# Optimization experiments

Hardware: AMD Instinct MI355X
Metric: run time of the kernel (lower is better)

Reference implementation:

```python
import jax, jax.numpy as jnp
import numpy as np

EPS = 1e-8

def squash(s, axis=-1):
    sq = jnp.sum(s * s, axis=axis, keepdims=True)
    return (sq / (1.0 + sq)) * s / jnp.sqrt(sq + EPS)

def conv3d(x, w, b, stride=1):
    y = jax.lax.conv_general_dilated(x, w, (stride,) * 3, 'VALID',
                                     dimension_numbers=('NCDHW', 'OIDHW', 'NCDHW'))
    return y + b[None, :, None, None, None]

def deconv3d(x, w, b, stride, pad, out_pad):
    # torch ConvTranspose3d: w is (Cin, Cout, k, k, k)
    k = w.shape[-1]
    wf = jnp.flip(w, axis=(2, 3, 4)).transpose(1, 0, 2, 3, 4)  # (Cout, Cin, k, k, k)
    pads = [(k - 1 - pad, k - 1 - pad + out_pad)] * 3
    y = jax.lax.conv_general_dilated(x, wf, (1, 1, 1), pads,
                                     lhs_dilation=(stride,) * 3,
                                     dimension_numbers=('NCDHW', 'OIDHW', 'NCDHW'))
    return y + b[None, :, None, None, None]

def voxel_ids(pcl, n):
    # per-cloud axis-aligned bounding box voxelization (PyntCloud voxelgrid semantics)
    mn = pcl.min(axis=1, keepdims=True)
    mx = pcl.max(axis=1, keepdims=True)
    idx = jnp.floor((pcl - mn) / (mx - mn + 1e-9) * n).astype(jnp.int32)
    idx = jnp.clip(idx, 0, n - 1)
    return idx[..., 0] * (n * n) + idx[..., 1] * n + idx[..., 2]  # (B, P) flat voxel id

def setup_inputs() -> dict:
    key = jax.random.key(0)
    ks = jax.random.split(key, 16)
    B, P, C, n = 2, 8192, 128, 24
    s = 0.02
    inp = {
        'pcl': jax.random.uniform(ks[0], (B, P, 3), jnp.float32),
        'pcl_feature': jax.random.normal(ks[1], (B, P, C), jnp.float32),
        'n': n,
        'conv1_w': jax.random.normal(ks[2], (256, 128, 5, 5, 5), jnp.float32) * s,
        'conv1_b': jnp.zeros((256,), jnp.float32),
        'conv2_w': jax.random.normal(ks[3], (256, 256, 5, 5, 5), jnp.float32) * s,
        'conv2_b': jnp.zeros((256,), jnp.float32),
        'prim_w': jax.random.normal(ks[4], (256, 256, 9, 9, 9), jnp.float32) * s,
        'prim_b': jnp.zeros((256,), jnp.float32),
        'route_w': jax.random.normal(ks[5], (50, 2048, 64, 8), jnp.float32) * s,
        'dec1_w': jax.random.normal(ks[6], (50, 128, 3, 3, 3), jnp.float32) * s,
        'dec1_b': jnp.zeros((128,), jnp.float32),
        'dec2_w': jax.random.normal(ks[7], (128, 512, 3, 3, 3), jnp.float32) * s,
        'dec2_b': jnp.zeros((512,), jnp.float32),
    }
    return inp

def reference(pcl, pcl_feature, n, conv1_w, conv1_b, conv2_w, conv2_b,
              prim_w, prim_b, route_w, dec1_w, dec1_b, dec2_w, dec2_b):
    B, P, C = pcl_feature.shape
    vid = voxel_ids(pcl, n)  # (B, P)
    # pcl2vox: scatter-add point features into dense voxel grid
    flat_ids = (jnp.arange(B)[:, None] * (n ** 3) + vid).reshape(-1)
    mesh = jax.ops.segment_sum(pcl_feature.reshape(B * P, C), flat_ids,
                               num_segments=B * n ** 3)
    mesh = mesh.reshape(B, n, n, n, C).transpose(0, 4, 1, 2, 3)  # (B, C, n, n, n)
    # conv encoder: 24 -> 20 -> 16
    h = jax.nn.relu(conv3d(mesh, conv1_w, conv1_b))
    h = jax.nn.relu(conv3d(h, conv2_w, conv2_b))  # (B, 256, 16, 16, 16)
    # primary capsules: k=9 s=2 -> (B, 256, 4, 4, 4) -> (B, 2048, 8), squash
    p = conv3d(h, prim_w, prim_b, stride=2)
    u = p.reshape(B, 32, 8, 64).transpose(0, 1, 3, 2).reshape(B, 2048, 8)
    u = squash(u)
    # dynamic routing: u_hat[b,j,i,d] = W[j,i,d,c] u[b,i,c]
    u_hat = jnp.einsum('jidc,bic->bjid', route_w, u)  # (B, 50, 2048, 64)
    b_log = jnp.zeros((B, 50, 2048), u_hat.dtype)
    n_iter = 1
    v = None
    for _ in range(n_iter):
        c = jax.nn.softmax(b_log, axis=1)
        s = jnp.einsum('bji,bjid->bjd', c, u_hat)
        v = squash(s)  # (B, 50, 64)
        b_log = b_log + jnp.einsum('bjid,bjd->bji', u_hat, v)
    # decoder: (B, 50, 4, 4, 4) -> (B, 128, 12^3) -> (B, 512, 24^3)
    r = v.reshape(B, 50, 4, 4, 4)
    d = jax.nn.relu(deconv3d(r, dec1_w, dec1_b, 3, 0, 0))
    d = jax.nn.relu(deconv3d(d, dec2_w, dec2_b, 2, 1, 1))  # (B, 512, 24, 24, 24)
    # vox2pcl: gather per-point features from voxel grid
    d_flat = d.reshape(B, 512, n ** 3)
    out = jnp.take_along_axis(d_flat, vid[:, None, :], axis=2)  # (B, 512, P)
    return out.transpose(0, 2, 1)  # (B, P, 512)
```

## Files before the change

### kernel.cpp

```cpp
#include <hip/hip_runtime.h>
#include <cstdint>
#include <cstddef>

typedef _Float16 h8 __attribute__((ext_vector_type(8)));
typedef _Float16 h4 __attribute__((ext_vector_type(4)));
typedef float    f32x4 __attribute__((ext_vector_type(4)));

#define B_   2
#define P_   8192
#define NVOX 24
#define N3   13824

#define MESHS_OFF 0ull
#define M16_OFF   14155776ull
#define H1CL_OFF  28311552ull
#define WB_OFF    44695552ull
#define WB2C_OFF  44695552ull
#define H2P_OFF   0ull
#define PPART_OFF 25165824ull
#define PR1_OFF   53477376ull
#define WBD_OFF   0ull
#define D2H_OFF   10616832ull
#define D1CL_OFF  38928384ull
#define VID_OFF   63504384ull
#define UBUF_OFF  63700992ull
#define SBUF_OFF  63832064ull
#define VBUF_OFF  63857664ull

#define M16_PL   3538944ull
#define H1_PL    4096000ull
#define D1_PL    442368ull

__device__ inline void split2(float x, _Float16& a0, _Float16& a1)
{
    a0 = (_Float16)x;
    float r = x - (float)a0;
    a1 = (_Float16)(r * 2048.0f);
}

__device__ inline void gload16(const void* g, void* l)
{
    __builtin_amdgcn_global_load_lds(
        (const __attribute__((address_space(1))) char*)g,
        (__attribute__((address_space(3))) char*)l, 16, 0, 0);
}

__device__ inline void tapDecode(int cls, int ti, int& kd, int& kh, int& kw)
{
    int px = (cls >> 2) & 1, py = (cls >> 1) & 1, pz = cls & 1;
    int tiz = pz ? (ti & 1) : 0;
    int t1  = ti >> pz;
    int tiy = py ? (t1 & 1) : 0;
    int tix = t1 >> py;
    kd = px ? tix*2 : 1;
    kh = py ? tiy*2 : 1;
    kw = pz ? tiz*2 : 1;
}

__global__ __launch_bounds__(256)
void k_vid(const float* __restrict__ pcl, int* __restrict__ vid)
{
    int b = blockIdx.x;
    const float* pb = pcl + (size_t)b * P_ * 3;
    float mn[3] = {3e38f, 3e38f, 3e38f};
    float mx[3] = {-3e38f, -3e38f, -3e38f};
    for (int p = threadIdx.x; p < P_; p += 256) {
        #pragma unroll
        for (int d = 0; d < 3; ++d) {
            float v = pb[p*3 + d];
            mn[d] = fminf(mn[d], v);
            mx[d] = fmaxf(mx[d], v);
        }
    }
    __shared__ float red[6][256];
    #pragma unroll
    for (int d = 0; d < 3; ++d) { red[d][threadIdx.x] = mn[d]; red[3+d][threadIdx.x] = mx[d]; }
    __syncthreads();
    for (int s = 128; s > 0; s >>= 1) {
        if (threadIdx.x < (unsigned)s) {
            #pragma unroll
            for (int d = 0; d < 3; ++d) {
                red[d][threadIdx.x]   = fminf(red[d][threadIdx.x],   red[d][threadIdx.x + s]);
                red[3+d][threadIdx.x] = fmaxf(red[3+d][threadIdx.x], red[3+d][threadIdx.x + s]);
            }
        }
        __syncthreads();
    }
    float mn0 = red[0][0], mn1 = red[1][0], mn2 = red[2][0];
    float dd0 = red[3][0] - mn0 + 1e-9f;
    float dd1 = red[4][0] - mn1 + 1e-9f;
    float dd2 = red[5][0] - mn2 + 1e-9f;
    for (int p = threadIdx.x; p < P_; p += 256) {
        float fx = (pb[p*3+0] - mn0) / dd0 * 24.0f;
        float fy = (pb[p*3+1] - mn1) / dd1 * 24.0f;
        float fz = (pb[p*3+2] - mn2) / dd2 * 24.0f;
        int ix = (int)floorf(fx); ix = ix < 0 ? 0 : (ix > 23 ? 23 : ix);
        int iy = (int)floorf(fy); iy = iy < 0 ? 0 : (iy > 23 ? 23 : iy);
        int iz = (int)floorf(fz); iz = iz < 0 ? 0 : (iz > 23 ? 23 : iz);
        vid[b*P_ + p] = ix*576 + iy*24 + iz;
    }
}

__global__ __launch_bounds__(256)
void k_scatter(const float* __restrict__ feat, const int* __restrict__ vid,
               float* __restrict__ meshS)
{
    int g = blockIdx.x*256 + threadIdx.x;
    int c  = g & 127;
    int bp = g >> 7;
    int v  = vid[bp];
    int b  = bp >> 13;
    atomicAdd(&meshS[((size_t)b*N3 + v)*128 + c], feat[g]);
}

__global__ __launch_bounds__(256)
void k_meshsplit(const float* __restrict__ meshS, _Float16* __restrict__ m16)
{
    int g = blockIdx.x*256 + threadIdx.x;
    int e = g*4;
    float4 a = *(const float4*)(meshS + e);
    h4 v0, v1;
    float xs[4] = {a.x, a.y, a.z, a.w};
    #pragma unroll
    for (int j = 0; j < 4; ++j) {
        _Float16 t0, t1; split2(xs[j], t0, t1);
        v0[j] = t0; v1[j] = t1;
    }
    *(h4*)(m16 + e)          = v0;
    *(h4*)(m16 + M16_PL + e) = v1;
}

__global__ __launch_bounds__(256)
void k_splitw1(const float* __restrict__ W, char* __restrict__ Wb)
{
    int g = blockIdx.x*256 + threadIdx.x;
    int el   = g & 8191;
    int tile = g >> 13;
    int m = tile / 250, c = tile - m*250;
    int co = el >> 6, kl = el & 63;
    int kg = c*64 + kl;
    int kid = kg >> 7, ci = kg & 127;
    float x = W[((size_t)((m*128 + co)*128 + ci))*125 + kid];
    _Float16 a0, a1; split2(x, a0, a1);
    char* dst = Wb + (size_t)tile*32768 + (co*128 + ((kl*2) ^ ((co&7)<<4)));
    *(_Float16*)(dst)         = a0;
    *(_Float16*)(dst + 16384) = a1;
}

__global__ __launch_bounds__(256)
void k_splitw2(const float* __restrict__ W, char* __restrict__ Wb, int cBase, int NC)
{
    int g = blockIdx.x*256 + threadIdx.x;
    int el   = g & 8191;
    int tile = g >> 13;
    int m = tile / NC, cl = tile - m*NC;
    int c = cBase + cl;
    int co = el >> 6, kl = el & 63;
    int kg = c*64 + kl;
    int kid = kg >> 8, ci = kg & 255;
    float x = W[((size_t)((m*128 + co)*256 + ci))*125 + kid];
    _Float16 a0, a1; split2(x, a0, a1);
    char* dst = Wb + (size_t)tile*32768 + (co*128 + ((kl*2) ^ ((co&7)<<4)));
    *(_Float16*)(dst)         = a0;
    *(_Float16*)(dst + 16384) = a1;
}

__global__ __launch_bounds__(256)
void k_splitwd2p(const float* __restrict__ W, char* __restrict__ Wb)
{
    int g = blockIdx.x*256 + threadIdx.x;
    int el   = g & 8191;
    int tile = g >> 13;
    int mG = tile / 54, chunkG = tile - mG*54;
    int co = el >> 6, kl = el & 63;
    int rem = chunkG, cls = 0;
    for (int c = 0; c < 8; ++c) {
        int cc = 2 << __popc(c);
        if (rem < cc) { cls = c; break; }
        rem -= cc;
    }
    int k  = rem*64 + kl;
    int ti = k >> 7;
    int ci = k & 127;
    int kd, kh, kw;
    tapDecode(cls, ti, kd, kh, kw);
    int kid = kd*9 + kh*3 + kw;
    float x = W[((size_t)ci*512 + (mG*128 + co))*27 + kid];
    _Float16 a0, a1; split2(x, a0, a1);
    char* dst = Wb + (size_t)tile*32768 + (co*128 + ((kl*2) ^ ((co&7)<<4)));
    *(_Float16*)(dst)         = a0;
    *(_Float16*)(dst + 16384) = a1;
}

__global__ __launch_bounds__(256, 3)
void k_conv1(const _Float16* __restrict__ m16, const char* __restrict__ Wb,
             const float* __restrict__ bias, _Float16* __restrict__ h1cl)
{
    extern __shared__ char lds[];
    const int tid = threadIdx.x;
    const int l   = tid & 63;
    const int w   = tid >> 6;
    const int wm  = w >> 1, wn = w & 1;
    const int n0  = blockIdx.x * 64;
    const int m   = blockIdx.y;

    const _Float16* preP[4];
    #pragma unroll
    for (int i = 0; i < 4; ++i) {
        int g   = w*4096 + i*1024 + l*16;
        int ver = g >> 13;
        int dd  = g & 8191;
        int nl  = dd >> 7;
        int lg  = (dd & 127) ^ ((nl & 7) << 4);
        int klocal = lg >> 1;
        int n  = n0 + nl;
        int b2 = n / 8000;
        int so = n - b2*8000;
        int x = so/400, y = (so/20)%20, z = so%20;
        preP[i] = m16 + (size_t)ver*M16_PL
                      + ((size_t)(b2*13824 + x*576 + y*24 + z))*128 + klocal;
    }

    const int swz = (l & 7) << 4;
    const int qo  = (l >> 4) << 4;
    const int plF = (l & 15)*128 + (qo ^ (swz & 0x30)) + (swz & 0x40);

    f32x4 acc0[4][2], acc1[4][2];
    const f32x4 zz = {0.f, 0.f, 0.f, 0.f};
    #pragma unroll
    for (int a = 0; a < 4; ++a)
        #pragma unroll
        for (int b = 0; b < 2; ++b) { acc0[a][b] = zz; acc1[a][b] = zz; }

    for (int c = 0; c < 250; ++c) {
        int kid = c >> 1;
        int kd = kid/25, rr = kid - kd*25, kh = rr/5, kw = rr - kh*5;
        int koff = (kd*576 + kh*24 + kw)*128 + (c & 1)*64;

        __syncthreads();
        {
            const char* wsrc = (const char*)Wb + ((size_t)(m*250 + c))*32768 + w*8192;
            #pragma unroll
            for (int i = 0; i < 8; ++i)
                gload16(wsrc + i*1024 + l*16, lds + w*8192 + i*1024);
            #pragma unroll
            for (int i = 0; i < 4; ++i)
                gload16(preP[i] + koff, lds + 32768 + w*4096 + i*1024);
        }
        __syncthreads();

        #pragma unroll
        for (int ks = 0; ks < 2; ++ks) {
            const int kx = ks ? 64 : 0;
            h8 af[2][4], bf[2][2];
            #pragma unroll
            for (int v = 0; v < 2; ++v) {
                #pragma unroll
                for (int mf = 0; mf < 4; ++mf)
                    af[v][mf] = *(const h8*)(lds + v*16384 + (wm*64 + mf*16)*128 + (plF ^ kx));
                #pragma unroll
                for (int nf = 0; nf < 2; ++nf)
                    bf[v][nf] = *(const h8*)(lds + 32768 + v*8192 + (wn*32 + nf*16)*128 + (plF ^ kx));
            }
            #pragma unroll
            for (int mf = 0; mf < 4; ++mf)
                #pragma unroll
                for (int nf = 0; nf < 2; ++nf) {
                    acc0[mf][nf] = __builtin_amdgcn_mfma_f32_16x16x32_f16(af[0][mf], bf[0][nf], acc0[mf][nf], 0,0,0);
                    acc1[mf][nf] = __builtin_amdgcn_mfma_f32_16x16x32_f16(af[0][mf], bf[1][nf], acc1[mf][nf], 0,0,0);
                    acc1[mf][nf] = __builtin_amdgcn_mfma_f32_16x16x32_f16(af[1][mf], bf[0][nf], acc1[mf][nf], 0,0,0);
                }
        }
    }

    const float s1 = 4.8828125e-04f;
    #pragma unroll
    for (int mf = 0; mf < 4; ++mf)
        #pragma unroll
        for (int nf = 0; nf < 2; ++nf) {
            f32x4 r = acc0[mf][nf] + s1*acc1[mf][nf];
            int co = m*128 + wm*64 + mf*16 + ((l>>4)<<2);
            int n  = n0 + wn*32 + nf*16 + (l&15);
            size_t base = (size_t)n*256 + co;
            h4 v0, v1;
            #pragma unroll
            for (int rr = 0; rr < 4; ++rr) {
                float x = fmaxf(r[rr] + bias[co + rr], 0.f);
                _Float16 t0, t1; split2(x, t0, t1);
                v0[rr] = t0; v1[rr] = t1;
            }
            *(h4*)(h1cl + base)         = v0;
            *(h4*)(h1cl + H1_PL + base) = v1;
        }
}

__global__ __launch_bounds__(256, 3)
void k_conv2(const _Float16* __restrict__ h1cl, const char* __restrict__ Wb,
             float* __restrict__ h2p, int cBase, int NSt, int accum)
{
    extern __shared__ char lds[];
    const int tid = threadIdx.x;
    const int l   = tid & 63;
    const int w   = tid >> 6;
    const int wm  = w >> 1, wn = w & 1;
    const int n0  = blockIdx.x * 64;
    const int m   = blockIdx.y;
    const int per = (NSt + (int)gridDim.z - 1) / (int)gridDim.z;
    const int cl0 = blockIdx.z * per;
    const int cl1 = min(NSt, cl0 + per);

    const _Float16* preP[4];
    #pragma unroll
    for (int i = 0; i < 4; ++i) {
        int g   = w*4096 + i*1024 + l*16;
        int ver = g >> 13;
        int dd  = g & 8191;
        int nl  = dd >> 7;
        int lg  = (dd & 127) ^ ((nl & 7) << 4);
        int klocal = lg >> 1;
        int n = n0 + nl;
        int b2 = n >> 12, so = n & 4095;
        int x = so >> 8, y = (so >> 4) & 15, z = so & 15;
        preP[i] = h1cl + (size_t)ver*H1_PL
                       + ((size_t)(b2*8000 + x*400 + y*20 + z))*256 + klocal;
    }

    const int swz = (l & 7) << 4;
    const int qo  = (l >> 4) << 4;
    const int plF = (l & 15)*128 + (qo ^ (swz & 0x30)) + (swz & 0x40);

    f32x4 acc0[4][2], acc1[4][2];
    const f32x4 zz = {0.f, 0.f, 0.f, 0.f};
    #pragma unroll
    for (int a = 0; a < 4; ++a)
        #pragma unroll
        for (int b = 0; b < 2; ++b) { acc0[a][b] = zz; acc1[a][b] = zz; }

    for (int cl = cl0; cl < cl1; ++cl) {
        int cg = cBase + cl;
        int kid = cg >> 2;
        int kd = kid/25, rr = kid - kd*25, kh = rr/5, kw = rr - kh*5;
        int koff = (kd*400 + kh*20 + kw)*256 + (cg & 3)*64;

        __syncthreads();
        {
            const char* wsrc = (const char*)Wb + ((size_t)(m*NSt + cl))*32768 + w*8192;
            #pragma unroll
            for (int i = 0; i < 8; ++i)
                gload16(wsrc + i*1024 + l*16, lds + w*8192 + i*1024);
            #pragma unroll
            for (int i = 0; i < 4; ++i)
                gload16(preP[i] + koff, lds + 32768 + w*4096 + i*1024);
        }
        __syncthreads();

        #pragma unroll
        for (int ks = 0; ks < 2; ++ks) {
            const int kx = ks ? 64 : 0;
            h8 af[2][4], bf[2][2];
            #pragma unroll
            for (int v = 0; v < 2; ++v) {
                #pragma unroll
                for (int mf = 0; mf < 4; ++mf)
                    af[v][mf] = *(const h8*)(lds + v*16384 + (wm*64 + mf*16)*128 + (plF ^ kx));
                #pragma unroll
                for (int nf = 0; nf < 2; ++nf)
                    bf[v][nf] = *(const h8*)(lds + 32768 + v*8192 + (wn*32 + nf*16)*128 + (plF ^ kx));
            }
            #pragma unroll
            for (int mf = 0; mf < 4; ++mf)
                #pragma unroll
                for (int nf = 0; nf < 2; ++nf) {
                    acc0[mf][nf] = __builtin_amdgcn_mfma_f32_16x16x32_f16(af[0][mf], bf[0][nf], acc0[mf][nf], 0,0,0);
                    acc1[mf][nf] = __builtin_amdgcn_mfma_f32_16x16x32_f16(af[0][mf], bf[1][nf], acc1[mf][nf], 0,0,0);
                    acc1[mf][nf] = __builtin_amdgcn_mfma_f32_16x16x32_f16(af[1][mf], bf[0][nf], acc1[mf][nf], 0,0,0);
                }
        }
    }

    const float s1 = 4.8828125e-04f;
    float* oz = h2p + (size_t)blockIdx.z * 2097152;
    #pragma unroll
    for (int mf = 0; mf < 4; ++mf)
        #pragma unroll
        for (int nf = 0; nf < 2; ++nf) {
            f32x4 r = acc0[mf][nf] + s1*acc1[mf][nf];
            int co = m*128 + wm*64 + mf*16 + ((l>>4)<<2);
            int n  = n0 + wn*32 + nf*16 + (l&15);
            int b2 = n >> 12, so = n & 4095;
            #pragma unroll
            for (int rr = 0; rr < 4; ++rr) {
                size_t idx = ((size_t)(b2*256 + co + rr))*4096 + so;
                if (accum) oz[idx] += r[rr];
                else       oz[idx]  = r[rr];
            }
        }
}

__global__ __launch_bounds__(256)
void k_h2epi(float* __restrict__ p0, const float* __restrict__ bias)
{
    int g = blockIdx.x*256 + threadIdx.x;
    int e = g*4;
    int co = (e >> 12) & 255;
    float4 a = *(const float4*)(p0 + e);
    float4 b = *(const float4*)(p0 + 2097152 + e);
    float4 c = *(const float4*)(p0 + 4194304 + e);
    float bb = bias[co];
    float4 r;
    r.x = fmaxf(a.x + b.x + c.x + bb, 0.f);
    r.y = fmaxf(a.y + b.y + c.y + bb, 0.f);
    r.z = fmaxf(a.z + b.z + c.z + bb, 0.f);
    r.w = fmaxf(a.w + b.w + c.w + bb, 0.f);
    *(float4*)(p0 + e) = r;
}

template<int CIN, int KD, int STRIDE, int IND, int OUTD>
__global__ __launch_bounds__(256, 2)
void k_gemm_conv(const float* __restrict__ in, const float* __restrict__ W,
                 float* __restrict__ out)
{
    constexpr int KD2  = KD*KD;
    constexpr int K3   = KD*KD*KD;
    constexpr int IND2 = IND*IND;
    constexpr int IND3 = IND2*IND;
    constexpr int OUT2 = OUTD*OUTD;
    constexpr int OUT3 = OUT2*OUTD;
    constexpr int KTOT = CIN*K3;
    constexpr int NCH  = KTOT/16;

    const int tid  = threadIdx.x;
    const int mIdx = tid >> 4;
    const int nIdx = tid & 15;
    const int n0   = blockIdx.x * 128;
    const int co0  = blockIdx.y * 128;
    const int per  = NCH / (int)gridDim.z;
    const int c0   = blockIdx.z * per;
    const int c1   = c0 + per;

    __shared__ float As[16][132];
    __shared__ float Bs[16][132];

    const int nB    = n0 + (tid & 127);
    const int kHalf = tid >> 7;
    int bB = nB / OUT3;
    int sB = nB - bB*OUT3;
    int xB = sB / OUT2;
    int yB = (sB / OUTD) % OUTD;
    int zB = sB % OUTD;
    const float* inB = in + (size_t)bB*CIN*IND3
                          + (xB*STRIDE)*IND2 + (yB*STRIDE)*IND + (zB*STRIDE);
    const int cB  = tid & 127;
    const int qB  = cB >> 2;
    const int bpos = ((((qB & 1) << 4) | (qB >> 1)) << 2) | (cB & 3);

    const int aCo = tid >> 2;
    const int aKq = (tid & 3) * 4;
    const int qA  = aCo >> 2;
    const int apos = ((((qA & 1) << 4) | (qA >> 1)) << 2) | (aCo & 3);
    const float* Wr0 = W + (size_t)(co0 + aCo)*KTOT + aKq;
    const float* Wr1 = W + (size_t)(co0 + 64 + aCo)*KTOT + aKq;

    float acc[8][8];
    #pragma unroll
    for (int i = 0; i < 8; ++i)
        #pragma unroll
        for (int j = 0; j < 8; ++j) acc[i][j] = 0.f;

    for (int c = c0; c < c1; ++c) {
        const int kb = c*16;
        float4 a0 = *(const float4*)(Wr0 + kb);
        float4 a1 = *(const float4*)(Wr1 + kb);
        float bv[8];
        #pragma unroll
        for (int p = 0; p < 8; ++p) {
            int k  = kb + p*2 + kHalf;
            int ci = k / K3;
            int r  = k - ci*K3;
            int kd = r / KD2;
            int r2 = r - kd*KD2;
            int kh = r2 / KD;
            int kw = r2 - kh*KD;
            bv[p] = inB[ci*IND3 + kd*IND2 + kh*IND + kw];
        }
        __syncthreads();
        As[aKq+0][apos] = a0.x; As[aKq+1][apos] = a0.y;
        As[aKq+2][apos] = a0.z; As[aKq+3][apos] = a0.w;
        As[aKq+0][apos+32] = a1.x; As[aKq+1][apos+32] = a1.y;
        As[aKq+2][apos+32] = a1.z; As[aKq+3][apos+32] = a1.w;
        #pragma unroll
        for (int p = 0; p < 8; ++p) Bs[p*2 + kHalf][bpos] = bv[p];
        __syncthreads();
        #pragma unroll
        for (int kk = 0; kk < 16; ++kk) {
            float af[8], bf[8];
            *(float4*)&af[0] = *(const float4*)&As[kk][mIdx*4];
            *(float4*)&af[4] = *(const float4*)&As[kk][64 + mIdx*4];
            *(float4*)&bf[0] = *(const float4*)&Bs[kk][nIdx*4];
            *(float4*)&bf[4] = *(const float4*)&Bs[kk][64 + nIdx*4];
            #pragma unroll
            for (int i = 0; i < 8; ++i)
                #pragma unroll
                for (int j = 0; j < 8; ++j)
                    acc[i][j] += af[i]*bf[j];
        }
    }

    float* oz = out + (size_t)blockIdx.z * (2*256*OUT3);
    #pragma unroll
    for (int j = 0; j < 8; ++j) {
        int n = n0 + nIdx*8 + j;
        int b = n / OUT3;
        int s = n - b*OUT3;
        float* o = oz + ((size_t)b*256 + co0 + mIdx*8)*OUT3 + s;
        #pragma unroll
        for (int i = 0; i < 8; ++i)
            o[(size_t)i*OUT3] = acc[i][j];
    }
}

__global__ __launch_bounds__(256)
void k_pr1(const float* __restrict__ pp, float* __restrict__ out1)
{
    int e = blockIdx.x*256 + threadIdx.x;
    int y = blockIdx.y;
    const float* src = pp + (size_t)y*27*32768 + e;
    float a = 0.f;
    #pragma unroll
    for (int j = 0; j < 27; ++j) a += src[(size_t)j*32768];
    out1[y*32768 + e] = a;
}

__global__ __launch_bounds__(256)
void k_pr2(const float* __restrict__ out1, const float* __restrict__ pbias,
           float* __restrict__ u)
{
    int g = blockIdx.x*256 + threadIdx.x;
    int b = g >> 11;
    int i = g & 2047;
    int cap = i >> 6;
    int s   = i & 63;
    float vals[8];
    float sq = 0.f;
    #pragma unroll
    for (int c = 0; c < 8; ++c) {
        size_t base = ((size_t)(b*256) + cap*8 + c)*64 + s;
        float a = 0.f;
        #pragma unroll
        for (int j = 0; j < 8; ++j) a += out1[(size_t)j*32768 + base];
        float x = a + pbias[cap*8 + c];
        vals[c] = x;
        sq += x*x;
    }
    float scale = (sq / (1.f + sq)) / sqrtf(sq + 1e-8f);
    #pragma unroll
    for (int c = 0; c < 8; ++c) u[(size_t)g*8 + c] = vals[c]*scale;
}

__global__ __launch_bounds__(256)
void k_route(const float* __restrict__ Wr, const float* __restrict__ u,
             float* __restrict__ s_buf)
{
    int j  = blockIdx.x;
    int i0 = blockIdx.y * 512;
    __shared__ float us[2*512*8];
    for (int idx = threadIdx.x; idx < 8192; idx += 256) {
        int b = idx >> 12;
        us[idx] = u[(size_t)b*16384 + (size_t)i0*8 + (idx & 4095)];
    }
    __syncthreads();
    int tid = threadIdx.x;
    int cc  = tid & 7;
    const float* Wj = Wr + (size_t)j*2048*512 + (size_t)i0*512;
    float a00 = 0.f, a01 = 0.f, a10 = 0.f, a11 = 0.f;
    for (int i = 0; i < 512; ++i) {
        float w0 = Wj[(size_t)i*512 + tid];
        float w1 = Wj[(size_t)i*512 + tid + 256];
        float u0 = us[i*8 + cc];
        float u1 = us[4096 + i*8 + cc];
        a00 += w0*u0; a01 += w1*u0; a10 += w0*u1; a11 += w1*u1;
    }
    __syncthreads();
    float* red = us;
    red[tid] = a00; red[256 + tid] = a01; red[512 + tid] = a10; red[768 + tid] = a11;
    __syncthreads();
    if (tid < 128) {
        int b = tid >> 6, d = tid & 63;
        const float* rb = red + b*512 + (d >> 5)*256 + (d & 31)*8;
        float s = 0.f;
        #pragma unroll
        for (int c2 = 0; c2 < 8; ++c2) s += rb[c2];
        atomicAdd(&s_buf[((size_t)b*50 + j)*64 + d], s * (1.0f/50.0f));
    }
}

__global__ __launch_bounds__(64)
void k_squash_v(const float* __restrict__ s_buf, float* __restrict__ v_buf)
{
    int row = blockIdx.x;
    int d   = threadIdx.x;
    float s  = s_buf[row*64 + d];
    float sq = s*s;
    #pragma unroll
    for (int o = 32; o > 0; o >>= 1) sq += __shfl_xor(sq, o);
    float scale = (sq / (1.f + sq)) / sqrtf(sq + 1e-8f);
    v_buf[row*64 + d] = s*scale;
}

__global__ __launch_bounds__(256)
void k_dec1(const float* __restrict__ v, const float* __restrict__ W,
            const float* __restrict__ bias, _Float16* __restrict__ d1cl)
{
    int g  = blockIdx.x*256 + threadIdx.x;
    int co = g & 127;
    int t  = g >> 7;
    int o  = t % 1728;
    int b  = t / 1728;
    int ox = o / 144, oy = (o/12) % 12, oz = o % 12;
    int ix = ox/3, ka = ox - 3*ix;
    int iy = oy/3, kb = oy - 3*iy;
    int iz = oz/3, kc = oz - 3*iz;
    int widx = ka*9 + kb*3 + kc;
    int sidx = ix*16 + iy*4 + iz;
    float s = 0.f;
    for (int ci = 0; ci < 50; ++ci)
        s += v[((size_t)b*50 + ci)*64 + sidx] * W[((size_t)ci*128 + co)*27 + widx];
    float x = fmaxf(s + bias[co], 0.f);
    _Float16 a0, a1; split2(x, a0, a1);
    size_t base = (size_t)(b*1728 + o)*128 + co;
    d1cl[base]         = a0;
    d1cl[base + D1_PL] = a1;
}

__global__ __launch_bounds__(256, 3)
void k_dec2p(const _Float16* __restrict__ d1cl, const char* __restrict__ Wb,
             const float* __restrict__ bias, float* __restrict__ out, int coBase)
{
    extern __shared__ char lds[];
    const int tid = threadIdx.x;
    const int l   = tid & 63;
    const int w   = tid >> 6;
    const int wm  = w >> 1, wn = w & 1;
    const int cls = blockIdx.z;
    const int px  = (cls >> 2) & 1, py = (cls >> 1) & 1, pz = cls & 1;
    const int n0  = blockIdx.x * 64;
    const int m   = blockIdx.y;
    const int mG  = (coBase >> 7) + m;

    int cb = 0;
    for (int c = 0; c < cls; ++c) cb += 2 << __popc(c);
    const int nch = 2 << __popc(cls);

    const int nRow = tid & 63;
    const int q    = tid >> 6;
    const int nT   = n0 + nRow;
    const int b2s  = nT / 1728;
    const int rs   = nT - b2s*1728;
    const int oxh  = rs/144, oyh = (rs/12)%12, ozh = rs%12;
    const int posB = b2s*1728;
    const int bw0 = 32768 + nRow*128 + ((q*32)      ^ ((nRow&7)<<4));
    const int bw1 = 32768 + nRow*128 + ((q*32 + 16) ^ ((nRow&7)<<4));

    const int swz = (l & 7) << 4;
    const int qo  = (l >> 4) << 4;
    const int plF = (l & 15)*128 + (qo ^ (swz & 0x30)) + (swz & 0x40);

    f32x4 acc0[4][2], acc1[4][2];
    const f32x4 zz = {0.f, 0.f, 0.f, 0.f};
    #pragma unroll
    for (int a = 0; a < 4; ++a)
        #pragma unroll
        for (int b = 0; b < 2; ++b) { acc0[a][b] = zz; acc1[a][b] = zz; }

    const h8 z8 = {};
    for (int c = 0; c < nch; ++c) {
        int ti = c >> 1, ch = c & 1;
        int kd, kh, kw;
        tapDecode(cls, ti, kd, kh, kw);
        int txh = oxh + (px && kd == 0);
        int tyh = oyh + (py && kh == 0);
        int tzh = ozh + (pz && kw == 0);
        bool ok = (txh < 12) && (tyh < 12) && (tzh < 12);
        const _Float16* src = d1cl + (size_t)(posB + txh*144 + tyh*12 + tzh)*128
                                   + ch*64 + q*16;
        h8 b0a = *(const h8*)(src);
        h8 b0b = *(const h8*)(src + 8);
        h8 b1a = *(const h8*)(src + D1_PL);
        h8 b1b = *(const h8*)(src + D1_PL + 8);

        __syncthreads();
        {
            const char* wsrc = (const char*)Wb + ((size_t)(mG*54 + cb + c))*32768 + w*8192;
            #pragma unroll
            for (int i = 0; i < 8; ++i)
                gload16(wsrc + i*1024 + l*16, lds + w*8192 + i*1024);
        }
        *(h8*)(lds + bw0)         = ok ? b0a : z8;
        *(h8*)(lds + bw1)         = ok ? b0b : z8;
        *(h8*)(lds + 8192 + bw0)  = ok ? b1a : z8;
        *(h8*)(lds + 8192 + bw1)  = ok ? b1b : z8;
        __syncthreads();

        #pragma unroll
        for (int ks = 0; ks < 2; ++ks) {
            const int kx = ks ? 64 : 0;
            h8 af[2][4], bf[2][2];
            #pragma unroll
            for (int v = 0; v < 2; ++v) {
                #pragma unroll
                for (int mf = 0; mf < 4; ++mf)
                    af[v][mf] = *(const h8*)(lds + v*16384 + (wm*64 + mf*16)*128 + (plF ^ kx));
                #pragma unroll
                for (int nf = 0; nf < 2; ++nf)
                    bf[v][nf] = *(const h8*)(lds + 32768 + v*8192 + (wn*32 + nf*16)*128 + (plF ^ kx));
            }
            #pragma unroll
            for (int mf = 0; mf < 4; ++mf)
                #pragma unroll
                for (int nf = 0; nf < 2; ++nf) {
                    acc0[mf][nf] = __builtin_amdgcn_mfma_f32_16x16x32_f16(af[0][mf], bf[0][nf], acc0[mf][nf], 0,0,0);
                    acc1[mf][nf] = __builtin_amdgcn_mfma_f32_16x16x32_f16(af[0][mf], bf[1][nf], acc1[mf][nf], 0,0,0);
                    acc1[mf][nf] = __builtin_amdgcn_mfma_f32_16x16x32_f16(af[1][mf], bf[0][nf], acc1[mf][nf], 0,0,0);
                }
        }
    }

    const float s1 = 4.8828125e-04f;
    #pragma unroll
    for (int mf = 0; mf < 4; ++mf)
        #pragma unroll
        for (int nf = 0; nf < 2; ++nf) {
            f32x4 r = acc0[mf][nf] + s1*acc1[mf][nf];
            int coL = m*128 + wm*64 + mf*16 + ((l>>4)<<2);
            int coG = coBase + coL;
            int nT2 = n0 + wn*32 + nf*16 + (l&15);
            int b2  = nT2 / 1728;
            int r2  = nT2 - b2*1728;
            int ax  = r2/144, ay = (r2/12)%12, az = r2%12;
            int outIdx = b2*13824 + (2*ax + px)*576 + (2*ay + py)*24 + (2*az + pz);
            float4 v;
            v.x = fmaxf(r[0] + bias[coG + 0], 0.f);
            v.y = fmaxf(r[1] + bias[coG + 1], 0.f);
            v.z = fmaxf(r[2] + bias[coG + 2], 0.f);
            v.w = fmaxf(r[3] + bias[coG + 3], 0.f);
            *(float4*)(out + (size_t)outIdx*256 + coL) = v;
        }
}

__global__ __launch_bounds__(256)
void k_gather(const float* __restrict__ d2h, const int* __restrict__ vid,
              float* __restrict__ out, int colOff)
{
    int g  = blockIdx.x*256 + threadIdx.x;
    int qq = g & 63;
    int bp = g >> 6;
    int v  = vid[bp];
    int b  = bp >> 13;
    float4 val = *(const float4*)&d2h[((size_t)(b*N3 + v))*256 + qq*4];
    *(float4*)&out[(size_t)bp*512 + colOff + qq*4] = val;
}

extern "C" void kernel_launch(void* const* d_in, const int* in_sizes, int n_in,
                              void* d_out, int out_size, void* d_ws, size_t ws_size,
                              hipStream_t stream)
{
    (void)in_sizes; (void)n_in; (void)out_size; (void)ws_size;
    const float* pcl  = (const float*)d_in[0];
    const float* feat = (const float*)d_in[1];
    const float* c1w  = (const float*)d_in[3];
    const float* c1b  = (const float*)d_in[4];
    const float* c2w  = (const float*)d_in[5];
    const float* c2b  = (const float*)d_in[6];
    const float* pw   = (const float*)d_in[7];
    const float* pb   = (const float*)d_in[8];
    const float* rw   = (const float*)d_in[9];
    const float* d1w  = (const float*)d_in[10];
    const float* d1b_ = (const float*)d_in[11];
    const float* d2w  = (const float*)d_in[12];
    const float* d2b  = (const float*)d_in[13];

    char* ws = (char*)d_ws;
    float*     meshS  = (float*)(ws + MESHS_OFF);
    _Float16*  m16    = (_Float16*)(ws + M16_OFF);
    _Float16*  h1cl   = (_Float16*)(ws + H1CL_OFF);
    char*      Wb     = ws + WB_OFF;
    char*      Wb2c   = ws + WB2C_OFF;
    float*     h2p    = (float*)(ws + H2P_OFF);
    float*     p_part = (float*)(ws + PPART_OFF);
    float*     pr1    = (float*)(ws + PR1_OFF);
    char*      Wbd    = ws + WBD_OFF;
    float*     d2h    = (float*)(ws + D2H_OFF);
    _Float16*  d1cl   = (_Float16*)(ws + D1CL_OFF);
    int*       vid    = (int*)(ws + VID_OFF);
    float*     u_buf  = (float*)(ws + UBUF_OFF);
    float*     s_buf  = (float*)(ws + SBUF_OFF);
    float*     v_buf  = (float*)(ws + VBUF_OFF);

    k_vid<<<dim3(B_), dim3(256), 0, stream>>>(pcl, vid);

    hipMemsetAsync(meshS, 0, 14155776, stream);
    k_scatter<<<dim3(8192), dim3(256), 0, stream>>>(feat, vid, meshS);
    k_meshsplit<<<dim3(3456), dim3(256), 0, stream>>>(meshS, m16);

    k_splitw1<<<dim3(16000), dim3(256), 0, stream>>>(c1w, Wb);
    k_conv1<<<dim3(250, 2), dim3(256), 49152, stream>>>(m16, Wb, c1b, h1cl);

    k_splitw2<<<dim3(15872), dim3(256), 0, stream>>>(c2w, Wb2c, 0, 248);
    k_conv2<<<dim3(128, 2, 3), dim3(256), 49152, stream>>>(h1cl, Wb2c, h2p, 0, 248, 0);
    k_splitw2<<<dim3(16128), dim3(256), 0, stream>>>(c2w, Wb2c, 248, 252);
    k_conv2<<<dim3(128, 2, 3), dim3(256), 49152, stream>>>(h1cl, Wb2c, h2p, 248, 252, 1);
    k_h2epi<<<dim3(2048), dim3(256), 0, stream>>>(h2p, c2b);

    k_gemm_conv<256,9,2,16,4><<<dim3(1, 2, 216), dim3(256), 0, stream>>>(h2p, pw, p_part);
    k_pr1<<<dim3(128, 8), dim3(256), 0, stream>>>(p_part, pr1);
    k_pr2<<<dim3(16), dim3(256), 0, stream>>>(pr1, pb, u_buf);

    hipMemsetAsync(s_buf, 0, 25600, stream);
    k_route<<<dim3(50, 4), dim3(256), 0, stream>>>(rw, u_buf, s_buf);
    k_squash_v<<<dim3(100), dim3(64), 0, stream>>>(s_buf, v_buf);

    k_dec1<<<dim3(1728), dim3(256), 0, stream>>>(v_buf, d1w, d1b_, d1cl);

    k_splitwd2p<<<dim3(6912), dim3(256), 0, stream>>>(d2w, Wbd);

    k_dec2p<<<dim3(54, 2, 8), dim3(256), 49152, stream>>>(d1cl, Wbd, d2b, d2h, 0);
    k_gather<<<dim3(4096), dim3(256), 0, stream>>>(d2h, vid, (float*)d_out, 0);
    k_dec2p<<<dim3(54, 2, 8), dim3(256), 49152, stream>>>(d1cl, Wbd, d2b, d2h, 256);
    k_gather<<<dim3(4096), dim3(256), 0, stream>>>(d2h, vid, (float*)d_out, 256);
}
```

Measured before the change: 1.359 ms.

## Run primary-capsule conv on MFMA with split-fp16 weights and channels-last input

Replaces the scalar FP32 tiled GEMM for the 9x9x9 stride-2 primary-capsule conv with an MFMA fp16 kernel that uses a two-term fp16 split of both operands to keep accuracy. The conv2 epilogue now also transposes to channels-last and splits into fp16 halves. Weights are repacked in five kernel-offset chunks so they fit in a reused workspace, with split-K over 64 z-blocks accumulated across chunks. This adds repacking kernels and extra launches in exchange for much higher matrix throughput.

```diff
diff --git a/kernel.cpp b/kernel.cpp
--- a/kernel.cpp
+++ b/kernel.cpp
@@ -17,11 +17,13 @@
 #define WB_OFF    44695552ull
 #define WB2C_OFF  44695552ull
 #define H2P_OFF   0ull
-#define PPART_OFF 25165824ull
-#define PR1_OFF   53477376ull
+#define IMG_OFF   0ull
+#define H2CL_OFF  39845888ull
+#define PPART_OFF 48234496ull
+#define PR1_OFF   56623104ull
 #define WBD_OFF   0ull
 #define D2H_OFF   10616832ull
-#define D1CL_OFF  38928384ull
+#define D1CL_OFF  41287680ull
 #define VID_OFF   63504384ull
 #define UBUF_OFF  63700992ull
 #define SBUF_OFF  63832064ull
@@ -29,6 +31,7 @@
 
 #define M16_PL   3538944ull
 #define H1_PL    4096000ull
+#define H2CL_PL  2097152ull
 #define D1_PL    442368ull
 
 __device__ inline void split2(float x, _Float16& a0, _Float16& a1)
@@ -192,6 +195,30 @@
     *(_Float16*)(dst + 16384) = a1;
 }
 
+__global__ __launch_bounds__(256)
+void k_wimg(const float* __restrict__ W, char* __restrict__ img,
+            int kidBase, int kids, int cps4)
+{
+    int col = threadIdx.x >> 6;
+    int cil = threadIdx.x & 63;
+    int coG = blockIdx.y >> 2;
+    int ciseg = blockIdx.y & 3;
+    int mG = blockIdx.z;
+    int co = coG*4 + col;
+    int ci = ciseg*64 + cil;
+    int kid0 = blockIdx.x * 16;
+    const float* src = W + ((size_t)((mG*128 + co)*256) + ci)*729 + kidBase + kid0;
+    int wbyte = co*128 + ((cil*2) ^ ((co&7)<<4));
+    int nk = min(16, kids - kid0);
+    for (int t = 0; t < nk; ++t) {
+        float x = src[t];
+        _Float16 a0, a1; split2(x, a0, a1);
+        char* dst = img + ((size_t)(mG*cps4 + (kid0+t)*4 + ciseg))*32768 + wbyte;
+        *(_Float16*)(dst)         = a0;
+        *(_Float16*)(dst + 16384) = a1;
+    }
+}
+
 __global__ __launch_bounds__(256, 3)
 void k_conv1(const _Float16* __restrict__ m16, const char* __restrict__ Wb,
              const float* __restrict__ bias, _Float16* __restrict__ h1cl)
@@ -398,125 +425,132 @@
 }
 
 __global__ __launch_bounds__(256)
-void k_h2epi(float* __restrict__ p0, const float* __restrict__ bias)
-{
-    int g = blockIdx.x*256 + threadIdx.x;
-    int e = g*4;
-    int co = (e >> 12) & 255;
-    float4 a = *(const float4*)(p0 + e);
-    float4 b = *(const float4*)(p0 + 2097152 + e);
-    float4 c = *(const float4*)(p0 + 4194304 + e);
-    float bb = bias[co];
-    float4 r;
-    r.x = fmaxf(a.x + b.x + c.x + bb, 0.f);
-    r.y = fmaxf(a.y + b.y + c.y + bb, 0.f);
-    r.z = fmaxf(a.z + b.z + c.z + bb, 0.f);
-    r.w = fmaxf(a.w + b.w + c.w + bb, 0.f);
-    *(float4*)(p0 + e) = r;
-}
-
-template<int CIN, int KD, int STRIDE, int IND, int OUTD>
-__global__ __launch_bounds__(256, 2)
-void k_gemm_conv(const float* __restrict__ in, const float* __restrict__ W,
-                 float* __restrict__ out)
-{
-    constexpr int KD2  = KD*KD;
-    constexpr int K3   = KD*KD*KD;
-    constexpr int IND2 = IND*IND;
-    constexpr int IND3 = IND2*IND;
-    constexpr int OUT2 = OUTD*OUTD;
-    constexpr int OUT3 = OUT2*OUTD;
-    constexpr int KTOT = CIN*K3;
-    constexpr int NCH  = KTOT/16;
-
-    const int tid  = threadIdx.x;
-    const int mIdx = tid >> 4;
-    const int nIdx = tid & 15;
-    const int n0   = blockIdx.x * 128;
-    const int co0  = blockIdx.y * 128;
-    const int per  = NCH / (int)gridDim.z;
-    const int c0   = blockIdx.z * per;
-    const int c1   = c0 + per;
-
-    __shared__ float As[16][132];
-    __shared__ float Bs[16][132];
-
-    const int nB    = n0 + (tid & 127);
-    const int kHalf = tid >> 7;
-    int bB = nB / OUT3;
-    int sB = nB - bB*OUT3;
-    int xB = sB / OUT2;
-    int yB = (sB / OUTD) % OUTD;
-    int zB = sB % OUTD;
-    const float* inB = in + (size_t)bB*CIN*IND3
-                          + (xB*STRIDE)*IND2 + (yB*STRIDE)*IND + (zB*STRIDE);
-    const int cB  = tid & 127;
-    const int qB  = cB >> 2;
-    const int bpos = ((((qB & 1) << 4) | (qB >> 1)) << 2) | (cB & 3);
-
-    const int aCo = tid >> 2;
-    const int aKq = (tid & 3) * 4;
-    const int qA  = aCo >> 2;
-    const int apos = ((((qA & 1) << 4) | (qA >> 1)) << 2) | (aCo & 3);
-    const float* Wr0 = W + (size_t)(co0 + aCo)*KTOT + aKq;
-    const float* Wr1 = W + (size_t)(co0 + 64 + aCo)*KTOT + aKq;
-
-    float acc[8][8];
-    #pragma unroll
-    for (int i = 0; i < 8; ++i)
-        #pragma unroll
-        for (int j = 0; j < 8; ++j) acc[i][j] = 0.f;
-
-    for (int c = c0; c < c1; ++c) {
-        const int kb = c*16;
-        float4 a0 = *(const float4*)(Wr0 + kb);
-        float4 a1 = *(const float4*)(Wr1 + kb);
-        float bv[8];
-        #pragma unroll
-        for (int p = 0; p < 8; ++p) {
-            int k  = kb + p*2 + kHalf;
-            int ci = k / K3;
-            int r  = k - ci*K3;
-            int kd = r / KD2;
-            int r2 = r - kd*KD2;
-            int kh = r2 / KD;
-            int kw = r2 - kh*KD;
-            bv[p] = inB[ci*IND3 + kd*IND2 + kh*IND + kw];
-        }
+void k_h2cl(const float* __restrict__ p0, const float* __restrict__ bias,
+            _Float16* __restrict__ h2cl)
+{
+    __shared__ float tile[32][33];
+    int b2  = blockIdx.z;
+    int so0 = blockIdx.x * 32;
+    int co0 = blockIdx.y * 32;
+    int i = threadIdx.x >> 5;
+    int j = threadIdx.x & 31;
+    #pragma unroll
+    for (int r = 0; r < 32; r += 8) {
+        size_t idx = ((size_t)(b2*256 + co0 + i + r))*4096 + so0 + j;
+        float v = p0[idx] + p0[2097152 + idx] + p0[4194304 + idx] + bias[co0 + i + r];
+        tile[i + r][j] = fmaxf(v, 0.f);
+    }
+    __syncthreads();
+    #pragma unroll
+    for (int r = 0; r < 32; r += 8) {
+        float x = tile[j][i + r];
+        _Float16 a0, a1; split2(x, a0, a1);
+        size_t o = ((size_t)(b2*4096 + so0 + i + r))*256 + co0 + j;
+        h2cl[o]           = a0;
+        h2cl[o + H2CL_PL] = a1;
+    }
+}
+
+__global__ __launch_bounds__(256, 3)
+void k_primm(const _Float16* __restrict__ h2cl, const char* __restrict__ Wb,
+             float* __restrict__ pp, int kidBase, int cps4, int accum)
+{
+    extern __shared__ char lds[];
+    const int tid = threadIdx.x;
+    const int l   = tid & 63;
+    const int w   = tid >> 6;
+    const int wm  = w >> 1, wn = w & 1;
+    const int n0  = blockIdx.x * 64;
+    const int m   = blockIdx.y;
+    const int per = (cps4 + 63) >> 6;
+    const int cl0 = blockIdx.z * per;
+    const int cl1 = min(cps4, cl0 + per);
+
+    const _Float16* preP[4];
+    #pragma unroll
+    for (int i = 0; i < 4; ++i) {
+        int g   = w*4096 + i*1024 + l*16;
+        int ver = g >> 13;
+        int dd  = g & 8191;
+        int nl  = dd >> 7;
+        int lg  = (dd & 127) ^ ((nl & 7) << 4);
+        int klocal = lg >> 1;
+        int n = n0 + nl;
+        int b2 = n >> 6, so = n & 63;
+        int x = so >> 4, y = (so >> 2) & 3, z = so & 3;
+        preP[i] = h2cl + (size_t)ver*H2CL_PL
+                       + ((size_t)(b2*4096 + x*512 + y*32 + z*2))*256 + klocal;
+    }
+
+    const int swz = (l & 7) << 4;
+    const int qo  = (l >> 4) << 4;
+    const int plF = (l & 15)*128 + (qo ^ (swz & 0x30)) + (swz & 0x40);
+
+    f32x4 acc0[4][2], acc1[4][2];
+    const f32x4 zz = {0.f, 0.f, 0.f, 0.f};
+    #pragma unroll
+    for (int a = 0; a < 4; ++a)
+        #pragma unroll
+        for (int b = 0; b < 2; ++b) { acc0[a][b] = zz; acc1[a][b] = zz; }
+
+    for (int cl = cl0; cl < cl1; ++cl) {
+        int kid = kidBase + (cl >> 2);
+        int kd = kid/81, rr = kid - kd*81, kh = rr/9, kw = rr - kh*9;
+        int koff = (kd*256 + kh*16 + kw)*256 + (cl & 3)*64;
+
         __syncthreads();
-        As[aKq+0][apos] = a0.x; As[aKq+1][apos] = a0.y;
-        As[aKq+2][apos] = a0.z; As[aKq+3][apos] = a0.w;
-        As[aKq+0][apos+32] = a1.x; As[aKq+1][apos+32] = a1.y;
-        As[aKq+2][apos+32] = a1.z; As[aKq+3][apos+32] = a1.w;
-        #pragma unroll
-        for (int p = 0; p < 8; ++p) Bs[p*2 + kHalf][bpos] = bv[p];
+        {
+            const char* wsrc = (const char*)Wb + ((size_t)(m*cps4 + cl))*32768 + w*8192;
+            #pragma unroll
+            for (int i = 0; i < 8; ++i)
+                gload16(wsrc + i*1024 + l*16, lds + w*8192 + i*1024);
+            #pragma unroll
+            for (int i = 0; i < 4; ++i)
+                gload16(preP[i] + koff, lds + 32768 + w*4096 + i*1024);
+        }
         __syncthreads();
-        #pragma unroll
-        for (int kk = 0; kk < 16; ++kk) {
-            float af[8], bf[8];
-            *(float4*)&af[0] = *(const float4*)&As[kk][mIdx*4];
-            *(float4*)&af[4] = *(const float4*)&As[kk][64 + mIdx*4];
-            *(float4*)&bf[0] = *(const float4*)&Bs[kk][nIdx*4];
-            *(float4*)&bf[4] = *(const float4*)&Bs[kk][64 + nIdx*4];
-            #pragma unroll
-            for (int i = 0; i < 8; ++i)
-                #pragma unroll
-                for (int j = 0; j < 8; ++j)
-                    acc[i][j] += af[i]*bf[j];
-        }
-    }
-
-    float* oz = out + (size_t)blockIdx.z * (2*256*OUT3);
-    #pragma unroll
-    for (int j = 0; j < 8; ++j) {
-        int n = n0 + nIdx*8 + j;
-        int b = n / OUT3;
-        int s = n - b*OUT3;
-        float* o = oz + ((size_t)b*256 + co0 + mIdx*8)*OUT3 + s;
-        #pragma unroll
-        for (int i = 0; i < 8; ++i)
-            o[(size_t)i*OUT3] = acc[i][j];
-    }
+
+        #pragma unroll
+        for (int ks = 0; ks < 2; ++ks) {
+            const int kx = ks ? 64 : 0;
+            h8 af[2][4], bf[2][2];
+            #pragma unroll
+            for (int v = 0; v < 2; ++v) {
+                #pragma unroll
+                for (int mf = 0; mf < 4; ++mf)
+                    af[v][mf] = *(const h8*)(lds + v*16384 + (wm*64 + mf*16)*128 + (plF ^ kx));
+                #pragma unroll
+                for (int nf = 0; nf < 2; ++nf)
+                    bf[v][nf] = *(const h8*)(lds + 32768 + v*8192 + (wn*32 + nf*16)*128 + (plF ^ kx));
+            }
+            #pragma unroll
+            for (int mf = 0; mf < 4; ++mf)
+                #pragma unroll
+                for (int nf = 0; nf < 2; ++nf) {
+                    acc0[mf][nf] = __builtin_amdgcn_mfma_f32_16x16x32_f16(af[0][mf], bf[0][nf], acc0[mf][nf], 0,0,0);
+                    acc1[mf][nf] = __builtin_amdgcn_mfma_f32_16x16x32_f16(af[0][mf], bf[1][nf], acc1[mf][nf], 0,0,0);
+                    acc1[mf][nf] = __builtin_amdgcn_mfma_f32_16x16x32_f16(af[1][mf], bf[0][nf], acc1[mf][nf], 0,0,0);
+                }
+        }
+    }
+
+    const float s1 = 4.8828125e-04f;
+    float* oz = pp + (size_t)blockIdx.z * 32768;
+    #pragma unroll
+    for (int mf = 0; mf < 4; ++mf)
+        #pragma unroll
+        for (int nf = 0; nf < 2; ++nf) {
+            f32x4 r = acc0[mf][nf] + s1*acc1[mf][nf];
+            int co = m*128 + wm*64 + mf*16 + ((l>>4)<<2);
+            int n  = n0 + wn*32 + nf*16 + (l&15);
+            int b2 = n >> 6, so = n & 63;
+            #pragma unroll
+            for (int rr = 0; rr < 4; ++rr) {
+                size_t idx = ((size_t)(b2*256 + co + rr))*64 + so;
+                if (accum) oz[idx] += r[rr];
+                else       oz[idx]  = r[rr];
+            }
+        }
 }
 
 __global__ __launch_bounds__(256)
@@ -524,10 +558,10 @@
 {
     int e = blockIdx.x*256 + threadIdx.x;
     int y = blockIdx.y;
-    const float* src = pp + (size_t)y*27*32768 + e;
+    const float* src = pp + (size_t)y*8*32768 + e;
     float a = 0.f;
     #pragma unroll
-    for (int j = 0; j < 27; ++j) a += src[(size_t)j*32768];
+    for (int j = 0; j < 8; ++j) a += src[(size_t)j*32768];
     out1[y*32768 + e] = a;
 }
 
@@ -786,6 +820,8 @@
     char*      Wb     = ws + WB_OFF;
     char*      Wb2c   = ws + WB2C_OFF;
     float*     h2p    = (float*)(ws + H2P_OFF);
+    char*      img    = ws + IMG_OFF;
+    _Float16*  h2cl   = (_Float16*)(ws + H2CL_OFF);
     float*     p_part = (float*)(ws + PPART_OFF);
     float*     pr1    = (float*)(ws + PR1_OFF);
     char*      Wbd    = ws + WBD_OFF;
@@ -809,9 +845,21 @@
     k_conv2<<<dim3(128, 2, 3), dim3(256), 49152, stream>>>(h1cl, Wb2c, h2p, 0, 248, 0);
     k_splitw2<<<dim3(16128), dim3(256), 0, stream>>>(c2w, Wb2c, 248, 252);
     k_conv2<<<dim3(128, 2, 3), dim3(256), 49152, stream>>>(h1cl, Wb2c, h2p, 248, 252, 1);
-    k_h2epi<<<dim3(2048), dim3(256), 0, stream>>>(h2p, c2b);
-
-    k_gemm_conv<256,9,2,16,4><<<dim3(1, 2, 216), dim3(256), 0, stream>>>(h2p, pw, p_part);
+
+    k_h2cl<<<dim3(128, 8, 2), dim3(256), 0, stream>>>(h2p, c2b, h2cl);
+
+    {
+        const int bases[5] = {0, 146, 292, 438, 584};
+        const int kidsA[5] = {146, 146, 146, 146, 145};
+        for (int s = 0; s < 5; ++s) {
+            int kids = kidsA[s];
+            int cps4 = kids * 4;
+            k_wimg<<<dim3((kids + 15)/16, 128, 2), dim3(256), 0, stream>>>(
+                pw, img, bases[s], kids, cps4);
+            k_primm<<<dim3(2, 2, 64), dim3(256), 49152, stream>>>(
+                h2cl, img, p_part, bases[s], cps4, s > 0);
+        }
+    }
     k_pr1<<<dim3(128, 8), dim3(256), 0, stream>>>(p_part, pr1);
     k_pr2<<<dim3(16), dim3(256), 0, stream>>>(pr1, pb, u_buf);
 
```

Measured after the change: 1.681 ms. 23.7% more time.
